# Kernel tuning notes

Measured on AMD Instinct MI355X. Metric: run time of the kernel, lower is better.

## Reference

```python
import jax, jax.numpy as jnp
import numpy as np

NUM_NEIGHBORS = 10


def setup_inputs() -> dict:
    key = jax.random.key(0)
    k1, k2, k3 = jax.random.split(key, 3)
    N, M, D, C = 2048, 131072, 256, 126
    features = jax.random.normal(k1, (N, D), dtype=jnp.float32)
    features_bank = jax.random.normal(k2, (M, D), dtype=jnp.float32)
    p = jax.random.uniform(k3, (M, C), dtype=jnp.float32)
    probs_bank = p / jnp.sum(p, axis=1, keepdims=True)  # rows are softmax probs
    return {"features": features, "features_bank": features_bank, "probs_bank": probs_bank}


def reference(features, features_bank, probs_bank):
    # soft k-nearest-neighbors pseudo-label refinement (euclidean cdist).
    # dist[n, m] = ||features[n] - features_bank[m]||_2
    q2 = jnp.sum(features * features, axis=1, keepdims=True)          # (N, 1)
    b2 = jnp.sum(features_bank * features_bank, axis=1)                # (M,)
    d2 = q2 - 2.0 * jnp.einsum('nd,md->nm', features, features_bank) + b2
    dist = jnp.sqrt(jnp.maximum(d2, 0.0))                              # (N, M)
    # torch: sort ascending, take first k  ==  top_k of negated distances
    _, idxs = jax.lax.top_k(-dist, NUM_NEIGHBORS)                      # (N, k)
    pred_probs = jnp.mean(probs_bank[idxs], axis=1)                    # (N, C)
    pred_labels = jnp.argmax(pred_probs, axis=1)                       # (N,)
    return pred_labels, pred_probs
```

## Files before the change

kernel.cpp:

```cpp
#include <hip/hip_runtime.h>

#define KNN 10
constexpr int N = 2048;
constexpr int M = 131072;
constexpr int D = 256;
constexpr int C = 126;

constexpr int BN = 128;
constexpr int BM = 128;
constexpr int NSUB = 8;
constexpr int NCHUNK = M / (BM * NSUB);
constexpr int CAND_PER_N = NCHUNK * KNN;
constexpr int KSEG = D / 32;
constexpr int STG = 32768;

typedef __fp16   half2v __attribute__((ext_vector_type(2)));
typedef _Float16 half8  __attribute__((ext_vector_type(8)));
typedef float   float4v __attribute__((ext_vector_type(4)));

typedef const __attribute__((address_space(1))) void* gas_p;
typedef __attribute__((address_space(3))) void* las_p;

__device__ __forceinline__ void gload_lds16(const void* g, void* l) {
  __builtin_amdgcn_global_load_lds((gas_p)g, (las_p)l, 16, 0, 0);
}

#define CHAIN(v, ix)                                                    \
  do {                                                                  \
    const bool c0 = (v) < s0, c1 = (v) < s1, c2 = (v) < s2,             \
               c3 = (v) < s3, c4_ = (v) < s4, c5 = (v) < s5,            \
               c6 = (v) < s6, c7 = (v) < s7, c8 = (v) < s8,             \
               c9 = (v) < s9;                                           \
    s9 = c8 ? s8 : (c9 ? (v) : s9); i9 = c8 ? i8 : (c9 ? (ix) : i9);    \
    s8 = c7 ? s7 : (c8 ? (v) : s8); i8 = c7 ? i7 : (c8 ? (ix) : i8);    \
    s7 = c6 ? s6 : (c7 ? (v) : s7); i7 = c6 ? i6 : (c7 ? (ix) : i7);    \
    s6 = c5 ? s5 : (c6 ? (v) : s6); i6 = c5 ? i5 : (c6 ? (ix) : i6);    \
    s5 = c4_ ? s4 : (c5 ? (v) : s5); i5 = c4_ ? i4 : (c5 ? (ix) : i5);  \
    s4 = c3 ? s3 : (c4_ ? (v) : s4); i4 = c3 ? i3 : (c4_ ? (ix) : i4);  \
    s3 = c2 ? s2 : (c3 ? (v) : s3); i3 = c2 ? i2 : (c3 ? (ix) : i3);    \
    s2 = c1 ? s1 : (c2 ? (v) : s2); i2 = c1 ? i1 : (c2 ? (ix) : i2);    \
    s1 = c0 ? s0 : (c1 ? (v) : s1); i1 = c0 ? i0 : (c1 ? (ix) : i1);    \
    s0 = c0 ? (v) : s0;             i0 = c0 ? (ix) : i0;                \
  } while (0)

__global__ __launch_bounds__(256) void b2_kernel(const float* __restrict__ bank,
                                                 float* __restrict__ b2) {
  const int wave = threadIdx.x >> 6, lane = threadIdx.x & 63;
  const int m = (blockIdx.x << 2) + wave;
  const float4 v = ((const float4*)(bank + (size_t)m * D))[lane];
  float s = v.x * v.x + v.y * v.y + v.z * v.z + v.w * v.w;
#pragma unroll
  for (int off = 32; off >= 1; off >>= 1) s += __shfl_down(s, off);
  if (lane == 0) b2[m] = s;
}

__global__ __launch_bounds__(256) void cvt_kernel(const float* __restrict__ src,
                                                  char* __restrict__ hi,
                                                  char* __restrict__ lo) {
  const int gid = blockIdx.x * 256 + threadIdx.x;
  const int m = gid >> 5, kg = gid & 31;
  const float4 v0 = *(const float4*)(src + (size_t)m * D + (kg << 3));
  const float4 v1 = *(const float4*)(src + (size_t)m * D + (kg << 3) + 4);
  union Pack { half2v h[4]; uint4 u; };
  Pack hh, ll;
  hh.h[0] = __builtin_amdgcn_cvt_pkrtz(v0.x, v0.y);
  hh.h[1] = __builtin_amdgcn_cvt_pkrtz(v0.z, v0.w);
  hh.h[2] = __builtin_amdgcn_cvt_pkrtz(v1.x, v1.y);
  hh.h[3] = __builtin_amdgcn_cvt_pkrtz(v1.z, v1.w);
  ll.h[0] = __builtin_amdgcn_cvt_pkrtz(v0.x - (float)hh.h[0].x, v0.y - (float)hh.h[0].y);
  ll.h[1] = __builtin_amdgcn_cvt_pkrtz(v0.z - (float)hh.h[1].x, v0.w - (float)hh.h[1].y);
  ll.h[2] = __builtin_amdgcn_cvt_pkrtz(v1.x - (float)hh.h[2].x, v1.y - (float)hh.h[2].y);
  ll.h[3] = __builtin_amdgcn_cvt_pkrtz(v1.z - (float)hh.h[3].x, v1.w - (float)hh.h[3].y);
  const size_t off = (((size_t)(m >> 4) * KSEG + (kg >> 2)) << 10) +
                     (((m & 15) | ((kg & 3) << 4)) << 4);
  *(uint4*)(hi + off) = hh.u;
  *(uint4*)(lo + off) = ll.u;
}

__global__ __launch_bounds__(256, 2) void knn_chunk_mfma(
    const char* __restrict__ pAhi, const char* __restrict__ pAlo,
    const char* __restrict__ pBhi, const char* __restrict__ pBlo,
    const float* __restrict__ b2g, float* __restrict__ cand_s,
    int* __restrict__ cand_i) {
  __shared__ char smem[65536];
  float* score = (float*)smem;
  char* stg = smem + STG;

  const int tid = threadIdx.x;
  const int lane = tid & 63;
  const int wave = tid >> 6;
  const int wx = wave & 1, wy = wave >> 1;
  const int n0 = blockIdx.y * BN;
  const int chunk = blockIdx.x;
  const int ag0 = n0 >> 4;

  float s0 = 3e38f, s1 = 3e38f, s2 = 3e38f, s3 = 3e38f, s4 = 3e38f,
        s5 = 3e38f, s6 = 3e38f, s7 = 3e38f, s8 = 3e38f, s9 = 3e38f;
  int i0 = -1, i1 = -1, i2 = -1, i3 = -1, i4 = -1,
      i5 = -1, i6 = -1, i7 = -1, i8 = -1, i9 = -1;

  auto stage = [&](int bg0, int kseg) {
#pragma unroll
    for (int t = 0; t < 2; ++t) {
      const int grp = (wave << 1) + t;
      const size_t aoff = (((size_t)(ag0 + grp) * KSEG + kseg) << 10) + (lane << 4);
      const size_t boff = (((size_t)(bg0 + grp) * KSEG + kseg) << 10) + (lane << 4);
      const int ldst = (grp << 10) + (lane << 4);
      gload_lds16(pAhi + aoff, stg + ldst);
      gload_lds16(pAlo + aoff, stg + 8192 + ldst);
      gload_lds16(pBhi + boff, stg + 16384 + ldst);
      gload_lds16(pBlo + boff, stg + 24576 + ldst);
    }
  };

  stage((chunk * NSUB) * BM >> 4, 0);

  for (int sub = 0; sub < NSUB; ++sub) {
    const int m0 = (chunk * NSUB + sub) * BM;
    const int bg0 = m0 >> 4;
    float4v acc[4][4];
#pragma unroll
    for (int i = 0; i < 4; ++i)
#pragma unroll
      for (int j = 0; j < 4; ++j) acc[i][j] = (float4v)(0.0f);

    for (int k = 0; k < KSEG; ++k) {
      __syncthreads();
      half8 ah[4], al[4], bh[4], bl[4];
#pragma unroll
      for (int t = 0; t < 4; ++t) {
        const int ao = (((wy << 2) + t) << 10) + (lane << 4);
        ah[t] = *(half8*)(stg + ao);
        al[t] = *(half8*)(stg + 8192 + ao);
        const int bo = (((wx << 2) + t) << 10) + (lane << 4);
        bh[t] = *(half8*)(stg + 16384 + bo);
        bl[t] = *(half8*)(stg + 24576 + bo);
      }
      __syncthreads();
      if (k < KSEG - 1) stage(bg0, k + 1);
      else if (sub < NSUB - 1) stage(bg0 + 8, 0);
#pragma unroll
      for (int i = 0; i < 4; ++i)
#pragma unroll
        for (int j = 0; j < 4; ++j) {
          acc[i][j] = __builtin_amdgcn_mfma_f32_16x16x32_f16(ah[i], bh[j], acc[i][j], 0, 0, 0);
          acc[i][j] = __builtin_amdgcn_mfma_f32_16x16x32_f16(ah[i], bl[j], acc[i][j], 0, 0, 0);
          acc[i][j] = __builtin_amdgcn_mfma_f32_16x16x32_f16(al[i], bh[j], acc[i][j], 0, 0, 0);
        }
    }

    float b2v[4];
#pragma unroll
    for (int j = 0; j < 4; ++j)
      b2v[j] = b2g[m0 + (wx << 6) + (j << 4) + (lane & 15)];

    for (int p = 0; p < 2; ++p) {
      __syncthreads();
      if (wy == p) {
#pragma unroll
        for (int i = 0; i < 4; ++i)
#pragma unroll
          for (int j = 0; j < 4; ++j) {
            const int colw = (wx << 6) + (j << 4) + (lane & 15);
#pragma unroll
            for (int r = 0; r < 4; ++r) {
              const int row = (i << 4) + ((lane >> 4) << 2) + r;
              score[(row << 7) + ((((colw >> 2) ^ (row & 31)) << 2) | (colw & 3))] =
                  fmaf(-2.0f, acc[i][j][r], b2v[j]);
            }
          }
      }
      __syncthreads();
      const int rr = tid & 127;
      if ((rr >> 6) == p) {
        const int lr = rr & 63;
        const int cbase = (tid >> 7) << 6;
        const float* srow = score + (lr << 7);
        const int key = lr & 31;
        const int cb4 = cbase >> 2;
#pragma unroll 4
        for (int g = 0; g < 16; ++g) {
          const float4 v = *(const float4*)(srow + (((cb4 + g) ^ key) << 2));
          const int ib = m0 + cbase + (g << 2);
          if (v.x < s9) CHAIN(v.x, ib);
          if (v.y < s9) CHAIN(v.y, ib + 1);
          if (v.z < s9) CHAIN(v.z, ib + 2);
          if (v.w < s9) CHAIN(v.w, ib + 3);
        }
      }
    }
  }

  __syncthreads();
  const int r = tid & 127, h = tid >> 7;
  float* mg = (float*)smem;
  if (h == 1) {
    float* p_ = mg + r * 20;
    p_[0] = s0; p_[1] = s1; p_[2] = s2; p_[3] = s3; p_[4] = s4;
    p_[5] = s5; p_[6] = s6; p_[7] = s7; p_[8] = s8; p_[9] = s9;
    int* q_ = (int*)(p_ + 10);
    q_[0] = i0; q_[1] = i1; q_[2] = i2; q_[3] = i3; q_[4] = i4;
    q_[5] = i5; q_[6] = i6; q_[7] = i7; q_[8] = i8; q_[9] = i9;
  }
  __syncthreads();
  if (h == 0) {
    const float* p_ = mg + r * 20;
    const int* q_ = (const int*)(p_ + 10);
#pragma unroll
    for (int q = 0; q < KNN; ++q) {
      const float v = p_[q];
      const int ix = q_[q];
      if (v < s9) CHAIN(v, ix);
    }
    const size_t base = ((size_t)(n0 + r) * NCHUNK + chunk) * KNN;
    cand_s[base + 0] = s0; cand_s[base + 1] = s1; cand_s[base + 2] = s2;
    cand_s[base + 3] = s3; cand_s[base + 4] = s4; cand_s[base + 5] = s5;
    cand_s[base + 6] = s6; cand_s[base + 7] = s7; cand_s[base + 8] = s8;
    cand_s[base + 9] = s9;
    cand_i[base + 0] = i0; cand_i[base + 1] = i1; cand_i[base + 2] = i2;
    cand_i[base + 3] = i3; cand_i[base + 4] = i4; cand_i[base + 5] = i5;
    cand_i[base + 6] = i6; cand_i[base + 7] = i7; cand_i[base + 8] = i8;
    cand_i[base + 9] = i9;
  }
}

__global__ __launch_bounds__(256, 2) void knn_chunk_fallback(
    const float* __restrict__ Ag, const float* __restrict__ Bg,
    const float* __restrict__ b2g, float* __restrict__ cand_s,
    int* __restrict__ cand_i) {
  __shared__ float smemf[64 * 130];
  char* lds = (char*)smemf;
  float (*S64)[130] = (float(*)[130])smemf;

  const int tid = threadIdx.x;
  const int lane = tid & 63;
  const int wave = tid >> 6;
  const int wx = wave & 1, wy = wave >> 1;
  const int n0 = blockIdx.y * BN;
  const int chunk = blockIdx.x;

  float ts[KNN];
  int ti_[KNN];
#pragma unroll
  for (int q = 0; q < KNN; ++q) { ts[q] = 3.0e38f; ti_[q] = -1; }

  for (int sub = 0; sub < NSUB; ++sub) {
    const int m0 = (chunk * NSUB + sub) * BM;
    float4v acc[4][4];
#pragma unroll
    for (int i = 0; i < 4; ++i)
#pragma unroll
      for (int j = 0; j < 4; ++j) acc[i][j] = (float4v)(0.0f);

    for (int k0 = 0; k0 < D; k0 += 32) {
      __syncthreads();
#pragma unroll
      for (int r = 0; r < 4; ++r) {
        const int id = tid + (r << 8);
        const int n = id >> 3;
        const int c4 = id & 7;
        const int k = c4 << 2;
        const int off = ((n >> 4) << 10) + (((n & 15) | ((k >> 3) << 4)) << 4) +
                        ((c4 & 1) << 3);
        {
          const float4 v = *(const float4*)(Ag + (size_t)(n0 + n) * D + k0 + k);
          const half2v h01 = __builtin_amdgcn_cvt_pkrtz(v.x, v.y);
          const half2v h23 = __builtin_amdgcn_cvt_pkrtz(v.z, v.w);
          const half2v l01 =
              __builtin_amdgcn_cvt_pkrtz(v.x - (float)h01.x, v.y - (float)h01.y);
          const half2v l23 =
              __builtin_amdgcn_cvt_pkrtz(v.z - (float)h23.x, v.w - (float)h23.y);
          union { half2v h[2]; uint2 u; } hh, ll;
          hh.h[0] = h01; hh.h[1] = h23;
          ll.h[0] = l01; ll.h[1] = l23;
          *(uint2*)(lds + off) = hh.u;
          *(uint2*)(lds + 8192 + off) = ll.u;
        }
        {
          const float4 v = *(const float4*)(Bg + (size_t)(m0 + n) * D + k0 + k);
          const half2v h01 = __builtin_amdgcn_cvt_pkrtz(v.x, v.y);
          const half2v h23 = __builtin_amdgcn_cvt_pkrtz(v.z, v.w);
          const half2v l01 =
              __builtin_amdgcn_cvt_pkrtz(v.x - (float)h01.x, v.y - (float)h01.y);
          const half2v l23 =
              __builtin_amdgcn_cvt_pkrtz(v.z - (float)h23.x, v.w - (float)h23.y);
          union { half2v h[2]; uint2 u; } hh, ll;
          hh.h[0] = h01; hh.h[1] = h23;
          ll.h[0] = l01; ll.h[1] = l23;
          *(uint2*)(lds + 16384 + off) = hh.u;
          *(uint2*)(lds + 24576 + off) = ll.u;
        }
      }
      __syncthreads();
      half8 ah[4], al[4], bh[4], bl[4];
#pragma unroll
      for (int t = 0; t < 4; ++t) {
        const int ao = ((((wy << 2) + t) << 10)) + (lane << 4);
        ah[t] = *(half8*)(lds + ao);
        al[t] = *(half8*)(lds + 8192 + ao);
        const int bo = ((((wx << 2) + t) << 10)) + (lane << 4);
        bh[t] = *(half8*)(lds + 16384 + bo);
        bl[t] = *(half8*)(lds + 24576 + bo);
      }
#pragma unroll
      for (int i = 0; i < 4; ++i)
#pragma unroll
        for (int j = 0; j < 4; ++j) {
          acc[i][j] = __builtin_amdgcn_mfma_f32_16x16x32_f16(ah[i], bh[j], acc[i][j], 0, 0, 0);
          acc[i][j] = __builtin_amdgcn_mfma_f32_16x16x32_f16(ah[i], bl[j], acc[i][j], 0, 0, 0);
          acc[i][j] = __builtin_amdgcn_mfma_f32_16x16x32_f16(al[i], bh[j], acc[i][j], 0, 0, 0);
        }
    }

    float b2v[4];
#pragma unroll
    for (int j = 0; j < 4; ++j)
      b2v[j] = b2g[m0 + (wx << 6) + (j << 4) + (lane & 15)];

    for (int p = 0; p < 2; ++p) {
      __syncthreads();
      if (wy == p) {
#pragma unroll
        for (int i = 0; i < 4; ++i)
#pragma unroll
          for (int j = 0; j < 4; ++j)
#pragma unroll
            for (int r = 0; r < 4; ++r)
              S64[(i << 4) + ((lane >> 4) << 2) + r]
                 [(wx << 6) + (j << 4) + (lane & 15)] =
                  fmaf(-2.0f, acc[i][j][r], b2v[j]);
      }
      __syncthreads();
      const int rr = tid & 127;
      if ((rr >> 6) == p) {
        const int lr = rr & 63;
        const int cbase = (tid >> 7) << 6;
        float cut = ts[KNN - 1];
        for (int c = 0; c < 64; ++c) {
          const float s = S64[lr][cbase + c];
          if (s < cut) {
            float cs = s;
            int ci = m0 + cbase + c;
#pragma unroll
            for (int q = 0; q < KNN; ++q) {
              if (cs < ts[q]) {
                const float tf = ts[q]; ts[q] = cs; cs = tf;
                const int tv = ti_[q]; ti_[q] = ci; ci = tv;
              }
            }
            cut = ts[KNN - 1];
          }
        }
      }
    }
  }

  __syncthreads();
  const int r = tid & 127, h = tid >> 7;
  float* mg = (float*)smemf;
  if (h == 1) {
#pragma unroll
    for (int q = 0; q < KNN; ++q) {
      mg[r * 20 + q] = ts[q];
      ((int*)mg)[r * 20 + 10 + q] = ti_[q];
    }
  }
  __syncthreads();
  if (h == 0) {
#pragma unroll
    for (int q = 0; q < KNN; ++q) {
      const float s = mg[r * 20 + q];
      const int idx = ((int*)mg)[r * 20 + 10 + q];
      if (s < ts[KNN - 1]) {
        float cs = s;
        int ci = idx;
#pragma unroll
        for (int u = 0; u < KNN; ++u) {
          if (cs < ts[u]) {
            const float tf = ts[u]; ts[u] = cs; cs = tf;
            const int tv = ti_[u]; ti_[u] = ci; ci = tv;
          }
        }
      }
    }
    const size_t base = ((size_t)(n0 + r) * NCHUNK + chunk) * KNN;
#pragma unroll
    for (int q = 0; q < KNN; ++q) {
      cand_s[base + q] = ts[q];
      cand_i[base + q] = ti_[q];
    }
  }
}

__global__ __launch_bounds__(256) void knn_finalize_kernel(
    const float* __restrict__ cand_s, const int* __restrict__ cand_i,
    const float* __restrict__ probs, float* __restrict__ out) {
  const int n = blockIdx.x, t = threadIdx.x;
  const size_t cb = (size_t)n * CAND_PER_N;

  float sc[5];
  int id_[5];
#pragma unroll
  for (int r = 0; r < 5; ++r) {
    sc[r] = cand_s[cb + t + (r << 8)];
    id_[r] = cand_i[cb + t + (r << 8)];
  }

  __shared__ float rs[4];
  __shared__ int rm[4];
  __shared__ int win[KNN];

  for (int round = 0; round < KNN; ++round) {
    float bs = 3.0e38f;
    int bm = 0x7fffffff;
#pragma unroll
    for (int r = 0; r < 5; ++r) {
      const bool better =
          (id_[r] >= 0) && (sc[r] < bs || (sc[r] == bs && id_[r] < bm));
      if (better) { bs = sc[r]; bm = id_[r]; }
    }
#pragma unroll
    for (int off = 32; off >= 1; off >>= 1) {
      const float os = __shfl_down(bs, off);
      const int om = __shfl_down(bm, off);
      if (os < bs || (os == bs && om < bm)) { bs = os; bm = om; }
    }
    if ((t & 63) == 0) { rs[t >> 6] = bs; rm[t >> 6] = bm; }
    __syncthreads();
    if (t == 0) {
      float fb = rs[0]; int fm = rm[0];
      for (int w = 1; w < 4; ++w)
        if (rs[w] < fb || (rs[w] == fb && rm[w] < fm)) { fb = rs[w]; fm = rm[w]; }
      win[round] = fm;
    }
    __syncthreads();
    const int wmv = win[round];
#pragma unroll
    for (int r = 0; r < 5; ++r)
      if (id_[r] == wmv) id_[r] = -1;
  }

  __shared__ float pv[128];
  float myp = -1.0e30f;
  if (t < C) {
    float acc = 0.0f;
#pragma unroll
    for (int q = 0; q < KNN; ++q) acc += probs[(size_t)win[q] * C + t];
    myp = acc * (1.0f / KNN);
    out[N + (size_t)n * C + t] = myp;
  }
  if (t < 128) pv[t] = myp;
  __syncthreads();
  if (t == 0) {
    float bv = pv[0];
    int bi = 0;
    for (int c = 1; c < C; ++c)
      if (pv[c] > bv) { bv = pv[c]; bi = c; }
    out[n] = (float)bi;
  }
}

extern "C" void kernel_launch(void* const* d_in, const int* in_sizes, int n_in,
                              void* d_out, int out_size, void* d_ws, size_t ws_size,
                              hipStream_t stream) {
  const float* features = (const float*)d_in[0];
  const float* bank = (const float*)d_in[1];
  const float* probs = (const float*)d_in[2];
  float* out = (float*)d_out;

  float* b2 = (float*)d_ws;
  float* cand_s = b2 + M;
  int* cand_i = (int*)(cand_s + (size_t)N * CAND_PER_N);
  char* Ahi = (char*)(cand_i + (size_t)N * CAND_PER_N);
  char* Alo = Ahi + (size_t)N * D * 2;
  char* Bhi = Alo + (size_t)N * D * 2;
  char* Blo = Bhi + (size_t)M * D * 2;
  const size_t NEED_FAST =
      (size_t)M * 4 + (size_t)N * CAND_PER_N * 8 + (size_t)N * D * 4 + (size_t)M * D * 4;

  b2_kernel<<<M / 4, 256, 0, stream>>>(bank, b2);
  if (ws_size >= NEED_FAST) {
    cvt_kernel<<<(N * 32) / 256, 256, 0, stream>>>(features, Ahi, Alo);
    cvt_kernel<<<(M * 32) / 256, 256, 0, stream>>>(bank, Bhi, Blo);
    knn_chunk_mfma<<<dim3(NCHUNK, N / BN), 256, 0, stream>>>(Ahi, Alo, Bhi, Blo,
                                                             b2, cand_s, cand_i);
  } else {
    knn_chunk_fallback<<<dim3(NCHUNK, N / BN), 256, 0, stream>>>(features, bank,
                                                                 b2, cand_s, cand_i);
  }
  knn_finalize_kernel<<<N, 256, 0, stream>>>(cand_s, cand_i, probs, out);
}
```

Baseline: 1.027 ms.

## Double-buffer LDS staging so async global loads overlap the MFMA steps

Splits shared memory into two 32 KB staging buffers. At each k-step the kernel issues the async global-to-LDS loads for the next step into the other buffer right after the barrier, then reads the current buffer. This removes one __syncthreads per step and lets the loads run while the MFMAs execute. The score scratch area now shares the second buffer, which is only safe because of the even/odd step parity, so the buffer use is more fragile.

```diff
diff --git a/kernel.cpp b/kernel.cpp
--- a/kernel.cpp
+++ b/kernel.cpp
@@ -12,7 +12,7 @@
 constexpr int NCHUNK = M / (BM * NSUB);
 constexpr int CAND_PER_N = NCHUNK * KNN;
 constexpr int KSEG = D / 32;
-constexpr int STG = 32768;
+constexpr int NSTEP = NSUB * KSEG;
 
 typedef __fp16   half2v __attribute__((ext_vector_type(2)));
 typedef _Float16 half8  __attribute__((ext_vector_type(8)));
@@ -83,8 +83,7 @@
     const float* __restrict__ b2g, float* __restrict__ cand_s,
     int* __restrict__ cand_i) {
   __shared__ char smem[65536];
-  float* score = (float*)smem;
-  char* stg = smem + STG;
+  float* score = (float*)(smem + 32768);
 
   const int tid = threadIdx.x;
   const int lane = tid & 63;
@@ -99,46 +98,48 @@
   int i0 = -1, i1 = -1, i2 = -1, i3 = -1, i4 = -1,
       i5 = -1, i6 = -1, i7 = -1, i8 = -1, i9 = -1;
 
-  auto stage = [&](int bg0, int kseg) {
-#pragma unroll
-    for (int t = 0; t < 2; ++t) {
-      const int grp = (wave << 1) + t;
-      const size_t aoff = (((size_t)(ag0 + grp) * KSEG + kseg) << 10) + (lane << 4);
-      const size_t boff = (((size_t)(bg0 + grp) * KSEG + kseg) << 10) + (lane << 4);
+  auto stage = [&](int tt) {
+    const int sb = tt >> 3, kk = tt & 7;
+    const int bg0 = (chunk * NSUB + sb) * (BM >> 4);
+    char* dst = smem + ((tt & 1) << 15);
+#pragma unroll
+    for (int t2 = 0; t2 < 2; ++t2) {
+      const int grp = (wave << 1) + t2;
+      const size_t aoff = (((size_t)(ag0 + grp) * KSEG + kk) << 10) + (lane << 4);
+      const size_t boff = (((size_t)(bg0 + grp) * KSEG + kk) << 10) + (lane << 4);
       const int ldst = (grp << 10) + (lane << 4);
-      gload_lds16(pAhi + aoff, stg + ldst);
-      gload_lds16(pAlo + aoff, stg + 8192 + ldst);
-      gload_lds16(pBhi + boff, stg + 16384 + ldst);
-      gload_lds16(pBlo + boff, stg + 24576 + ldst);
+      gload_lds16(pAhi + aoff, dst + ldst);
+      gload_lds16(pAlo + aoff, dst + 8192 + ldst);
+      gload_lds16(pBhi + boff, dst + 16384 + ldst);
+      gload_lds16(pBlo + boff, dst + 24576 + ldst);
     }
   };
 
-  stage((chunk * NSUB) * BM >> 4, 0);
-
+  stage(0);
+
+  int t = 0;
   for (int sub = 0; sub < NSUB; ++sub) {
     const int m0 = (chunk * NSUB + sub) * BM;
-    const int bg0 = m0 >> 4;
     float4v acc[4][4];
 #pragma unroll
     for (int i = 0; i < 4; ++i)
 #pragma unroll
       for (int j = 0; j < 4; ++j) acc[i][j] = (float4v)(0.0f);
 
-    for (int k = 0; k < KSEG; ++k) {
-      __syncthreads();
+    for (int k = 0; k < KSEG; ++k, ++t) {
+      __syncthreads();
+      if (t < NSTEP - 1) stage(t + 1);
+      const char* rb = smem + ((t & 1) << 15);
       half8 ah[4], al[4], bh[4], bl[4];
 #pragma unroll
-      for (int t = 0; t < 4; ++t) {
-        const int ao = (((wy << 2) + t) << 10) + (lane << 4);
-        ah[t] = *(half8*)(stg + ao);
-        al[t] = *(half8*)(stg + 8192 + ao);
-        const int bo = (((wx << 2) + t) << 10) + (lane << 4);
-        bh[t] = *(half8*)(stg + 16384 + bo);
-        bl[t] = *(half8*)(stg + 24576 + bo);
-      }
-      __syncthreads();
-      if (k < KSEG - 1) stage(bg0, k + 1);
-      else if (sub < NSUB - 1) stage(bg0 + 8, 0);
+      for (int q = 0; q < 4; ++q) {
+        const int ao = (((wy << 2) + q) << 10) + (lane << 4);
+        ah[q] = *(const half8*)(rb + ao);
+        al[q] = *(const half8*)(rb + 8192 + ao);
+        const int bo = (((wx << 2) + q) << 10) + (lane << 4);
+        bh[q] = *(const half8*)(rb + 16384 + bo);
+        bl[q] = *(const half8*)(rb + 24576 + bo);
+      }
 #pragma unroll
       for (int i = 0; i < 4; ++i)
 #pragma unroll
@@ -154,9 +155,9 @@
     for (int j = 0; j < 4; ++j)
       b2v[j] = b2g[m0 + (wx << 6) + (j << 4) + (lane & 15)];
 
-    for (int p = 0; p < 2; ++p) {
-      __syncthreads();
-      if (wy == p) {
+    for (int pp = 0; pp < 2; ++pp) {
+      __syncthreads();
+      if (wy == pp) {
 #pragma unroll
         for (int i = 0; i < 4; ++i)
 #pragma unroll
@@ -172,7 +173,7 @@
       }
       __syncthreads();
       const int rr = tid & 127;
-      if ((rr >> 6) == p) {
+      if ((rr >> 6) == pp) {
         const int lr = rr & 63;
         const int cbase = (tid >> 7) << 6;
         const float* srow = score + (lr << 7);
@@ -294,13 +295,13 @@
       __syncthreads();
       half8 ah[4], al[4], bh[4], bl[4];
 #pragma unroll
-      for (int t = 0; t < 4; ++t) {
-        const int ao = ((((wy << 2) + t) << 10)) + (lane << 4);
-        ah[t] = *(half8*)(lds + ao);
-        al[t] = *(half8*)(lds + 8192 + ao);
-        const int bo = ((((wx << 2) + t) << 10)) + (lane << 4);
-        bh[t] = *(half8*)(lds + 16384 + bo);
-        bl[t] = *(half8*)(lds + 24576 + bo);
+      for (int q = 0; q < 4; ++q) {
+        const int ao = ((((wy << 2) + q) << 10)) + (lane << 4);
+        ah[q] = *(half8*)(lds + ao);
+        al[q] = *(half8*)(lds + 8192 + ao);
+        const int bo = ((((wx << 2) + q) << 10)) + (lane << 4);
+        bh[q] = *(half8*)(lds + 16384 + bo);
+        bl[q] = *(half8*)(lds + 24576 + bo);
       }
 #pragma unroll
       for (int i = 0; i < 4; ++i)
```

Result: slower. 1.225 ms (+19.3%).

## Load query tile directly from global, shrink LDS to raise occupancy to 3

Applied to the files above, without the earlier changes.

The main kNN MFMA kernel no longer stages the pre-split hi/lo query (A) tiles through LDS. Each wave now reads its A fragments straight from global memory every k-step, where they should mostly hit in cache because every block reuses the same query rows. Only the bank (B) tiles stay in LDS, so the shared allocation drops from 64KB to 48KB. Launch bounds are raised to 3 blocks per CU to use the freed space. The cost is that the A global loads sit on the critical path without prefetching, and the tighter register budget may cause spills with the 64-float accumulator.

```diff
diff --git a/kernel.cpp b/kernel.cpp
--- a/kernel.cpp
+++ b/kernel.cpp
@@ -77,12 +77,12 @@
   *(uint4*)(lo + off) = ll.u;
 }
 
-__global__ __launch_bounds__(256, 2) void knn_chunk_mfma(
+__global__ __launch_bounds__(256, 3) void knn_chunk_mfma(
     const char* __restrict__ pAhi, const char* __restrict__ pAlo,
     const char* __restrict__ pBhi, const char* __restrict__ pBlo,
     const float* __restrict__ b2g, float* __restrict__ cand_s,
     int* __restrict__ cand_i) {
-  __shared__ char smem[65536];
+  __shared__ char smem[49152];
   float* score = (float*)smem;
   char* stg = smem + STG;
 
@@ -101,15 +101,12 @@
 
   auto stage = [&](int bg0, int kseg) {
 #pragma unroll
-    for (int t = 0; t < 2; ++t) {
-      const int grp = (wave << 1) + t;
-      const size_t aoff = (((size_t)(ag0 + grp) * KSEG + kseg) << 10) + (lane << 4);
+    for (int t2 = 0; t2 < 2; ++t2) {
+      const int grp = (wave << 1) + t2;
       const size_t boff = (((size_t)(bg0 + grp) * KSEG + kseg) << 10) + (lane << 4);
       const int ldst = (grp << 10) + (lane << 4);
-      gload_lds16(pAhi + aoff, stg + ldst);
-      gload_lds16(pAlo + aoff, stg + 8192 + ldst);
-      gload_lds16(pBhi + boff, stg + 16384 + ldst);
-      gload_lds16(pBlo + boff, stg + 24576 + ldst);
+      gload_lds16(pBhi + boff, stg + ldst);
+      gload_lds16(pBlo + boff, stg + 8192 + ldst);
     }
   };
 
@@ -126,15 +123,20 @@
 
     for (int k = 0; k < KSEG; ++k) {
       __syncthreads();
-      half8 ah[4], al[4], bh[4], bl[4];
+      half8 ah[4], al[4];
 #pragma unroll
       for (int t = 0; t < 4; ++t) {
-        const int ao = (((wy << 2) + t) << 10) + (lane << 4);
-        ah[t] = *(half8*)(stg + ao);
-        al[t] = *(half8*)(stg + 8192 + ao);
+        const size_t aoff =
+            (((size_t)(ag0 + (wy << 2) + t) * KSEG + k) << 10) + (lane << 4);
+        ah[t] = *(const half8*)(pAhi + aoff);
+        al[t] = *(const half8*)(pAlo + aoff);
+      }
+      half8 bh[4], bl[4];
+#pragma unroll
+      for (int t = 0; t < 4; ++t) {
         const int bo = (((wx << 2) + t) << 10) + (lane << 4);
-        bh[t] = *(half8*)(stg + 16384 + bo);
-        bl[t] = *(half8*)(stg + 24576 + bo);
+        bh[t] = *(half8*)(stg + bo);
+        bl[t] = *(half8*)(stg + 8192 + bo);
       }
       __syncthreads();
       if (k < KSEG - 1) stage(bg0, k + 1);
@@ -154,9 +156,9 @@
     for (int j = 0; j < 4; ++j)
       b2v[j] = b2g[m0 + (wx << 6) + (j << 4) + (lane & 15)];
 
-    for (int p = 0; p < 2; ++p) {
-      __syncthreads();
-      if (wy == p) {
+    for (int pp = 0; pp < 2; ++pp) {
+      __syncthreads();
+      if (wy == pp) {
 #pragma unroll
         for (int i = 0; i < 4; ++i)
 #pragma unroll
@@ -172,7 +174,7 @@
       }
       __syncthreads();
       const int rr = tid & 127;
-      if ((rr >> 6) == p) {
+      if ((rr >> 6) == pp) {
         const int lr = rr & 63;
         const int cbase = (tid >> 7) << 6;
         const float* srow = score + (lr << 7);
@@ -294,13 +296,13 @@
       __syncthreads();
       half8 ah[4], al[4], bh[4], bl[4];
 #pragma unroll
-      for (int t = 0; t < 4; ++t) {
-        const int ao = ((((wy << 2) + t) << 10)) + (lane << 4);
-        ah[t] = *(half8*)(lds + ao);
-        al[t] = *(half8*)(lds + 8192 + ao);
-        const int bo = ((((wx << 2) + t) << 10)) + (lane << 4);
-        bh[t] = *(half8*)(lds + 16384 + bo);
-        bl[t] = *(half8*)(lds + 24576 + bo);
+      for (int q = 0; q < 4; ++q) {
+        const int ao = ((((wy << 2) + q) << 10)) + (lane << 4);
+        ah[q] = *(half8*)(lds + ao);
+        al[q] = *(half8*)(lds + 8192 + ao);
+        const int bo = ((((wx << 2) + q) << 10)) + (lane << 4);
+        bh[q] = *(half8*)(lds + 16384 + bo);
+        bl[q] = *(half8*)(lds + 24576 + bo);
       }
 #pragma unroll
       for (int i = 0; i < 4; ++i)
```

New measurement: 2.571 ms. +150.4%, slower.

## Split top-k scan across all four waves and fuse bank norms into conversion

Applied to the files above, without the earlier changes.

Previously only half of the block's threads ran the serial top-k insertion chain in each score pass, two threads per row with 64 columns each. Now all 256 threads take part in every pass, four per row with 32 columns each, and each thread keeps two separate top-10 lists (one per row half), which are merged through shared memory at the end. The bank squared-norm computation is folded into the fp16 hi/lo conversion kernel, removing a separate pass over the bank. In exchange, the doubled per-thread top-k state raises register pressure and the final merge gains extra synchronisation and a longer reduction.

```diff
diff --git a/kernel.cpp b/kernel.cpp
--- a/kernel.cpp
+++ b/kernel.cpp
@@ -25,22 +25,32 @@
   __builtin_amdgcn_global_load_lds((gas_p)g, (las_p)l, 16, 0, 0);
 }
 
-#define CHAIN(v, ix)                                                    \
-  do {                                                                  \
-    const bool c0 = (v) < s0, c1 = (v) < s1, c2 = (v) < s2,             \
-               c3 = (v) < s3, c4_ = (v) < s4, c5 = (v) < s5,            \
-               c6 = (v) < s6, c7 = (v) < s7, c8 = (v) < s8,             \
-               c9 = (v) < s9;                                           \
-    s9 = c8 ? s8 : (c9 ? (v) : s9); i9 = c8 ? i8 : (c9 ? (ix) : i9);    \
-    s8 = c7 ? s7 : (c8 ? (v) : s8); i8 = c7 ? i7 : (c8 ? (ix) : i8);    \
-    s7 = c6 ? s6 : (c7 ? (v) : s7); i7 = c6 ? i6 : (c7 ? (ix) : i7);    \
-    s6 = c5 ? s5 : (c6 ? (v) : s6); i6 = c5 ? i5 : (c6 ? (ix) : i6);    \
-    s5 = c4_ ? s4 : (c5 ? (v) : s5); i5 = c4_ ? i4 : (c5 ? (ix) : i5);  \
-    s4 = c3 ? s3 : (c4_ ? (v) : s4); i4 = c3 ? i3 : (c4_ ? (ix) : i4);  \
-    s3 = c2 ? s2 : (c3 ? (v) : s3); i3 = c2 ? i2 : (c3 ? (ix) : i3);    \
-    s2 = c1 ? s1 : (c2 ? (v) : s2); i2 = c1 ? i1 : (c2 ? (ix) : i2);    \
-    s1 = c0 ? s0 : (c1 ? (v) : s1); i1 = c0 ? i0 : (c1 ? (ix) : i1);    \
-    s0 = c0 ? (v) : s0;             i0 = c0 ? (ix) : i0;                \
+#define CHAIN_P(P, v, ix)                                                    \
+  do {                                                                       \
+    const bool c0 = (v) < P##s0, c1 = (v) < P##s1, c2 = (v) < P##s2,         \
+               c3 = (v) < P##s3, c4_ = (v) < P##s4, c5 = (v) < P##s5,        \
+               c6 = (v) < P##s6, c7 = (v) < P##s7, c8 = (v) < P##s8,         \
+               c9 = (v) < P##s9;                                             \
+    P##s9 = c8 ? P##s8 : (c9 ? (v) : P##s9);                                 \
+    P##i9 = c8 ? P##i8 : (c9 ? (ix) : P##i9);                                \
+    P##s8 = c7 ? P##s7 : (c8 ? (v) : P##s8);                                 \
+    P##i8 = c7 ? P##i7 : (c8 ? (ix) : P##i8);                                \
+    P##s7 = c6 ? P##s6 : (c7 ? (v) : P##s7);                                 \
+    P##i7 = c6 ? P##i6 : (c7 ? (ix) : P##i7);                                \
+    P##s6 = c5 ? P##s5 : (c6 ? (v) : P##s6);                                 \
+    P##i6 = c5 ? P##i5 : (c6 ? (ix) : P##i6);                                \
+    P##s5 = c4_ ? P##s4 : (c5 ? (v) : P##s5);                                \
+    P##i5 = c4_ ? P##i4 : (c5 ? (ix) : P##i5);                               \
+    P##s4 = c3 ? P##s3 : (c4_ ? (v) : P##s4);                                \
+    P##i4 = c3 ? P##i3 : (c4_ ? (ix) : P##i4);                               \
+    P##s3 = c2 ? P##s2 : (c3 ? (v) : P##s3);                                 \
+    P##i3 = c2 ? P##i2 : (c3 ? (ix) : P##i3);                                \
+    P##s2 = c1 ? P##s1 : (c2 ? (v) : P##s2);                                 \
+    P##i2 = c1 ? P##i1 : (c2 ? (ix) : P##i2);                                \
+    P##s1 = c0 ? P##s0 : (c1 ? (v) : P##s1);                                 \
+    P##i1 = c0 ? P##i0 : (c1 ? (ix) : P##i1);                                \
+    P##s0 = c0 ? (v) : P##s0;                                                \
+    P##i0 = c0 ? (ix) : P##i0;                                               \
   } while (0)
 
 __global__ __launch_bounds__(256) void b2_kernel(const float* __restrict__ bank,
@@ -56,7 +66,8 @@
 
 __global__ __launch_bounds__(256) void cvt_kernel(const float* __restrict__ src,
                                                   char* __restrict__ hi,
-                                                  char* __restrict__ lo) {
+                                                  char* __restrict__ lo,
+                                                  float* __restrict__ b2) {
   const int gid = blockIdx.x * 256 + threadIdx.x;
   const int m = gid >> 5, kg = gid & 31;
   const float4 v0 = *(const float4*)(src + (size_t)m * D + (kg << 3));
@@ -75,6 +86,13 @@
                      (((m & 15) | ((kg & 3) << 4)) << 4);
   *(uint4*)(hi + off) = hh.u;
   *(uint4*)(lo + off) = ll.u;
+  if (b2 != nullptr) {
+    float s = v0.x * v0.x + v0.y * v0.y + v0.z * v0.z + v0.w * v0.w +
+              v1.x * v1.x + v1.y * v1.y + v1.z * v1.z + v1.w * v1.w;
+#pragma unroll
+    for (int o = 16; o >= 1; o >>= 1) s += __shfl_xor(s, o);
+    if (kg == 0) b2[m] = s;
+  }
 }
 
 __global__ __launch_bounds__(256, 2) void knn_chunk_mfma(
@@ -94,10 +112,14 @@
   const int chunk = blockIdx.x;
   const int ag0 = n0 >> 4;
 
-  float s0 = 3e38f, s1 = 3e38f, s2 = 3e38f, s3 = 3e38f, s4 = 3e38f,
-        s5 = 3e38f, s6 = 3e38f, s7 = 3e38f, s8 = 3e38f, s9 = 3e38f;
-  int i0 = -1, i1 = -1, i2 = -1, i3 = -1, i4 = -1,
-      i5 = -1, i6 = -1, i7 = -1, i8 = -1, i9 = -1;
+  float As0 = 3e38f, As1 = 3e38f, As2 = 3e38f, As3 = 3e38f, As4 = 3e38f,
+        As5 = 3e38f, As6 = 3e38f, As7 = 3e38f, As8 = 3e38f, As9 = 3e38f;
+  int Ai0 = -1, Ai1 = -1, Ai2 = -1, Ai3 = -1, Ai4 = -1,
+      Ai5 = -1, Ai6 = -1, Ai7 = -1, Ai8 = -1, Ai9 = -1;
+  float Bs0 = 3e38f, Bs1 = 3e38f, Bs2 = 3e38f, Bs3 = 3e38f, Bs4 = 3e38f,
+        Bs5 = 3e38f, Bs6 = 3e38f, Bs7 = 3e38f, Bs8 = 3e38f, Bs9 = 3e38f;
+  int Bi0 = -1, Bi1 = -1, Bi2 = -1, Bi3 = -1, Bi4 = -1,
+      Bi5 = -1, Bi6 = -1, Bi7 = -1, Bi8 = -1, Bi9 = -1;
 
   auto stage = [&](int bg0, int kseg) {
 #pragma unroll
@@ -154,9 +176,10 @@
     for (int j = 0; j < 4; ++j)
       b2v[j] = b2g[m0 + (wx << 6) + (j << 4) + (lane & 15)];
 
-    for (int p = 0; p < 2; ++p) {
-      __syncthreads();
-      if (wy == p) {
+#pragma unroll
+    for (int pp = 0; pp < 2; ++pp) {
+      __syncthreads();
+      if (wy == pp) {
 #pragma unroll
         for (int i = 0; i < 4; ++i)
 #pragma unroll
@@ -171,56 +194,96 @@
           }
       }
       __syncthreads();
-      const int rr = tid & 127;
-      if ((rr >> 6) == p) {
-        const int lr = rr & 63;
-        const int cbase = (tid >> 7) << 6;
+      {
+        const int lr = tid & 63;
+        const int qd = tid >> 6;
         const float* srow = score + (lr << 7);
         const int key = lr & 31;
-        const int cb4 = cbase >> 2;
+        const int cb4 = qd << 3;
 #pragma unroll 4
-        for (int g = 0; g < 16; ++g) {
+        for (int g = 0; g < 8; ++g) {
           const float4 v = *(const float4*)(srow + (((cb4 + g) ^ key) << 2));
-          const int ib = m0 + cbase + (g << 2);
-          if (v.x < s9) CHAIN(v.x, ib);
-          if (v.y < s9) CHAIN(v.y, ib + 1);
-          if (v.z < s9) CHAIN(v.z, ib + 2);
-          if (v.w < s9) CHAIN(v.w, ib + 3);
-        }
-      }
-    }
-  }
-
-  __syncthreads();
-  const int r = tid & 127, h = tid >> 7;
+          const int ib = m0 + (qd << 5) + (g << 2);
+          if (pp == 0) {
+            if (v.x < As9) CHAIN_P(A, v.x, ib);
+            if (v.y < As9) CHAIN_P(A, v.y, ib + 1);
+            if (v.z < As9) CHAIN_P(A, v.z, ib + 2);
+            if (v.w < As9) CHAIN_P(A, v.w, ib + 3);
+          } else {
+            if (v.x < Bs9) CHAIN_P(B, v.x, ib);
+            if (v.y < Bs9) CHAIN_P(B, v.y, ib + 1);
+            if (v.z < Bs9) CHAIN_P(B, v.z, ib + 2);
+            if (v.w < Bs9) CHAIN_P(B, v.w, ib + 3);
+          }
+        }
+      }
+    }
+  }
+
+  __syncthreads();
   float* mg = (float*)smem;
-  if (h == 1) {
-    float* p_ = mg + r * 20;
-    p_[0] = s0; p_[1] = s1; p_[2] = s2; p_[3] = s3; p_[4] = s4;
-    p_[5] = s5; p_[6] = s6; p_[7] = s7; p_[8] = s8; p_[9] = s9;
+  {
+    float* p_ = mg + tid * 20;
+    p_[0] = As0; p_[1] = As1; p_[2] = As2; p_[3] = As3; p_[4] = As4;
+    p_[5] = As5; p_[6] = As6; p_[7] = As7; p_[8] = As8; p_[9] = As9;
     int* q_ = (int*)(p_ + 10);
-    q_[0] = i0; q_[1] = i1; q_[2] = i2; q_[3] = i3; q_[4] = i4;
-    q_[5] = i5; q_[6] = i6; q_[7] = i7; q_[8] = i8; q_[9] = i9;
-  }
-  __syncthreads();
-  if (h == 0) {
-    const float* p_ = mg + r * 20;
-    const int* q_ = (const int*)(p_ + 10);
-#pragma unroll
-    for (int q = 0; q < KNN; ++q) {
-      const float v = p_[q];
-      const int ix = q_[q];
-      if (v < s9) CHAIN(v, ix);
-    }
-    const size_t base = ((size_t)(n0 + r) * NCHUNK + chunk) * KNN;
-    cand_s[base + 0] = s0; cand_s[base + 1] = s1; cand_s[base + 2] = s2;
-    cand_s[base + 3] = s3; cand_s[base + 4] = s4; cand_s[base + 5] = s5;
-    cand_s[base + 6] = s6; cand_s[base + 7] = s7; cand_s[base + 8] = s8;
-    cand_s[base + 9] = s9;
-    cand_i[base + 0] = i0; cand_i[base + 1] = i1; cand_i[base + 2] = i2;
-    cand_i[base + 3] = i3; cand_i[base + 4] = i4; cand_i[base + 5] = i5;
-    cand_i[base + 6] = i6; cand_i[base + 7] = i7; cand_i[base + 8] = i8;
-    cand_i[base + 9] = i9;
+    q_[0] = Ai0; q_[1] = Ai1; q_[2] = Ai2; q_[3] = Ai3; q_[4] = Ai4;
+    q_[5] = Ai5; q_[6] = Ai6; q_[7] = Ai7; q_[8] = Ai8; q_[9] = Ai9;
+  }
+  __syncthreads();
+  if (tid < 64) {
+#pragma unroll
+    for (int qd = 1; qd < 4; ++qd) {
+      const float* p_ = mg + ((qd << 6) + tid) * 20;
+      const int* q_ = (const int*)(p_ + 10);
+#pragma unroll
+      for (int q = 0; q < KNN; ++q) {
+        const float v = p_[q];
+        const int ix = q_[q];
+        if (v < As9) CHAIN_P(A, v, ix);
+      }
+    }
+    const size_t base = ((size_t)(n0 + tid) * NCHUNK + chunk) * KNN;
+    cand_s[base + 0] = As0; cand_s[base + 1] = As1; cand_s[base + 2] = As2;
+    cand_s[base + 3] = As3; cand_s[base + 4] = As4; cand_s[base + 5] = As5;
+    cand_s[base + 6] = As6; cand_s[base + 7] = As7; cand_s[base + 8] = As8;
+    cand_s[base + 9] = As9;
+    cand_i[base + 0] = Ai0; cand_i[base + 1] = Ai1; cand_i[base + 2] = Ai2;
+    cand_i[base + 3] = Ai3; cand_i[base + 4] = Ai4; cand_i[base + 5] = Ai5;
+    cand_i[base + 6] = Ai6; cand_i[base + 7] = Ai7; cand_i[base + 8] = Ai8;
+    cand_i[base + 9] = Ai9;
+  }
+  __syncthreads();
+  {
+    float* p_ = mg + tid * 20;
+    p_[0] = Bs0; p_[1] = Bs1; p_[2] = Bs2; p_[3] = Bs3; p_[4] = Bs4;
+    p_[5] = Bs5; p_[6] = Bs6; p_[7] = Bs7; p_[8] = Bs8; p_[9] = Bs9;
+    int* q_ = (int*)(p_ + 10);
+    q_[0] = Bi0; q_[1] = Bi1; q_[2] = Bi2; q_[3] = Bi3; q_[4] = Bi4;
+    q_[5] = Bi5; q_[6] = Bi6; q_[7] = Bi7; q_[8] = Bi8; q_[9] = Bi9;
+  }
+  __syncthreads();
+  if (tid < 64) {
+#pragma unroll
+    for (int qd = 1; qd < 4; ++qd) {
+      const float* p_ = mg + ((qd << 6) + tid) * 20;
+      const int* q_ = (const int*)(p_ + 10);
+#pragma unroll
+      for (int q = 0; q < KNN; ++q) {
+        const float v = p_[q];
+        const int ix = q_[q];
+        if (v < Bs9) CHAIN_P(B, v, ix);
+      }
+    }
+    const size_t base = ((size_t)(n0 + 64 + tid) * NCHUNK + chunk) * KNN;
+    cand_s[base + 0] = Bs0; cand_s[base + 1] = Bs1; cand_s[base + 2] = Bs2;
+    cand_s[base + 3] = Bs3; cand_s[base + 4] = Bs4; cand_s[base + 5] = Bs5;
+    cand_s[base + 6] = Bs6; cand_s[base + 7] = Bs7; cand_s[base + 8] = Bs8;
+    cand_s[base + 9] = Bs9;
+    cand_i[base + 0] = Bi0; cand_i[base + 1] = Bi1; cand_i[base + 2] = Bi2;
+    cand_i[base + 3] = Bi3; cand_i[base + 4] = Bi4; cand_i[base + 5] = Bi5;
+    cand_i[base + 6] = Bi6; cand_i[base + 7] = Bi7; cand_i[base + 8] = Bi8;
+    cand_i[base + 9] = Bi9;
   }
 }
 
@@ -294,13 +357,13 @@
       __syncthreads();
       half8 ah[4], al[4], bh[4], bl[4];
 #pragma unroll
-      for (int t = 0; t < 4; ++t) {
-        const int ao = ((((wy << 2) + t) << 10)) + (lane << 4);
-        ah[t] = *(half8*)(lds + ao);
-        al[t] = *(half8*)(lds + 8192 + ao);
-        const int bo = ((((wx << 2) + t) << 10)) + (lane << 4);
-        bh[t] = *(half8*)(lds + 16384 + bo);
-        bl[t] = *(half8*)(lds + 24576 + bo);
+      for (int q = 0; q < 4; ++q) {
+        const int ao = ((((wy << 2) + q) << 10)) + (lane << 4);
+        ah[q] = *(half8*)(lds + ao);
+        al[q] = *(half8*)(lds + 8192 + ao);
+        const int bo = ((((wx << 2) + q) << 10)) + (lane << 4);
+        bh[q] = *(half8*)(lds + 16384 + bo);
+        bl[q] = *(half8*)(lds + 24576 + bo);
       }
 #pragma unroll
       for (int i = 0; i < 4; ++i)
@@ -478,13 +541,13 @@
   const size_t NEED_FAST =
       (size_t)M * 4 + (size_t)N * CAND_PER_N * 8 + (size_t)N * D * 4 + (size_t)M * D * 4;
 
-  b2_kernel<<<M / 4, 256, 0, stream>>>(bank, b2);
   if (ws_size >= NEED_FAST) {
-    cvt_kernel<<<(N * 32) / 256, 256, 0, stream>>>(features, Ahi, Alo);
-    cvt_kernel<<<(M * 32) / 256, 256, 0, stream>>>(bank, Bhi, Blo);
+    cvt_kernel<<<(N * 32) / 256, 256, 0, stream>>>(features, Ahi, Alo, nullptr);
+    cvt_kernel<<<(M * 32) / 256, 256, 0, stream>>>(bank, Bhi, Blo, b2);
     knn_chunk_mfma<<<dim3(NCHUNK, N / BN), 256, 0, stream>>>(Ahi, Alo, Bhi, Blo,
                                                              b2, cand_s, cand_i);
   } else {
+    b2_kernel<<<M / 4, 256, 0, stream>>>(bank, b2);
     knn_chunk_fallback<<<dim3(NCHUNK, N / BN), 256, 0, stream>>>(features, bank,
                                                                  b2, cand_s, cand_i);
   }
```

New measurement: 970.6 us, median of 2. 5.5% less time.
